# Optimization experiments

Measured on AMD Instinct MI355X. Metric: run time of the kernel, lower is better.

## Reference

```python
import jax, jax.numpy as jnp
import numpy as np

N_NODES = 1_000_000
N_EDGES = 16_000_000
NUM_GRAPHS = 64
LATENT = 128
LAMBDA_LAP = 0.1
LAMBDA_DRIFT = 0.01
LAMBDA_ARAP = 0.1
BETA_WARMUP = 10
BETA_FINAL = 1.0


def setup_inputs() -> dict:
    key = jax.random.key(0)
    k1, k2, k3, k4, k5, k6 = jax.random.split(key, 6)
    return {
        "pred_output": jax.random.normal(k1, (N_NODES, 2), dtype=jnp.float32),
        "target": jax.random.normal(k2, (N_NODES, 2), dtype=jnp.float32),
        "edge_index": jax.random.randint(k3, (2, N_EDGES), 0, N_NODES, dtype=jnp.int32),
        "batch_indices": jnp.sort(jax.random.randint(k4, (N_NODES,), 0, NUM_GRAPHS, dtype=jnp.int32)),
        "mu": jax.random.normal(k5, (NUM_GRAPHS, LATENT), dtype=jnp.float32),
        "logvar": jax.random.normal(k6, (NUM_GRAPHS, LATENT), dtype=jnp.float32),
        "epoch": 5,
    }


def reference(pred_output, target, edge_index, batch_indices, mu, logvar, epoch):
    # reconstruction: MSE, mean over all elements
    recon = jnp.mean((pred_output - target) ** 2)

    # edge gather once; laplacian and ARAP reuse the same diff tensor
    i, j = edge_index[0], edge_index[1]
    diff = pred_output[i] - pred_output[j]                 # [E, 2]
    lap = jnp.sum(diff ** 2) / edge_index.shape[1]

    # drift suppression: per-graph mean displacement via segment_sum
    ones = jnp.ones((pred_output.shape[0],), dtype=pred_output.dtype)
    sums = jax.ops.segment_sum(pred_output, batch_indices, num_segments=NUM_GRAPHS)
    counts = jax.ops.segment_sum(ones, batch_indices, num_segments=NUM_GRAPHS)
    means = sums / counts[:, None]                         # [G, 2]
    drift = jnp.sum(means ** 2) / NUM_GRAPHS

    # ARAP: unbiased variance of edge lengths (torch.var default ddof=1)
    edge_len = jnp.sqrt(jnp.sum(diff ** 2, axis=1))        # [E]
    arap = jnp.var(edge_len, ddof=1)

    # KL divergence, mean over graphs
    kl = jnp.mean(-0.5 * jnp.sum(1.0 + logvar - mu ** 2 - jnp.exp(logvar), axis=1))

    # beta warmup (epoch is a static python int)
    beta = (epoch / BETA_WARMUP) * BETA_FINAL if epoch < BETA_WARMUP else BETA_FINAL

    total = recon + LAMBDA_LAP * lap + LAMBDA_DRIFT * drift + LAMBDA_ARAP * arap + beta * kl
    return total
```

## Files before the change

kernel.cpp:

```cpp
#include <hip/hip_runtime.h>
#include <hip/hip_fp16.h>
#include <math.h>

#define N_NODES    1000000
#define N_EDGES    16000000
#define NUM_GRAPHS 64
#define LATENT     128

#define NODE_BLOCKS 512
#define EDGE_BLOCKS 2048

#define EDGE_PART_OFF  0
#define RECON_PART_OFF 32768
#define KL_PART_OFF    36864
#define GSUM_PART_OFF  36872
#define PACKED_OFF     458752
#define WS_NEEDED      (PACKED_OFF + 4ull * N_NODES)

typedef int vint4 __attribute__((ext_vector_type(4)));

__global__ void node_kl_pass(const float2* __restrict__ pred,
                             const float2* __restrict__ targ,
                             const int*    __restrict__ batch,
                             const float*  __restrict__ mu,
                             const float*  __restrict__ logvar,
                             double* __restrict__ recon_part,
                             double* __restrict__ kl_part,
                             float*  __restrict__ gsum_part,
                             unsigned* __restrict__ packed) {
    __shared__ float sgx[NUM_GRAPHS];
    __shared__ float sgy[NUM_GRAPHS];
    __shared__ int   scnt[NUM_GRAPHS];
    __shared__ double smem[8];

    for (int g = threadIdx.x; g < NUM_GRAPHS; g += blockDim.x) {
        sgx[g] = 0.f; sgy[g] = 0.f; scnt[g] = 0;
    }
    __syncthreads();

    float recon = 0.f;
    const int idx = blockIdx.x * blockDim.x + threadIdx.x;
    const int stride = gridDim.x * blockDim.x;
    for (int n = idx; n < N_NODES; n += stride) {
        float2 p = pred[n];
        float2 t = targ[n];
        float dx = p.x - t.x, dy = p.y - t.y;
        recon += dx * dx + dy * dy;

        if (packed) {
            __half2 h = __floats2half2_rn(p.x, p.y);
            packed[n] = *reinterpret_cast<unsigned*>(&h);
        }

        int b = batch[n];
        unsigned long long act = __ballot(1);
        int b0 = __shfl(b, 0);
        bool fast = (act == ~0ull) && (__ballot(b == b0) == act);
        if (fast) {
            float sx = p.x, sy = p.y;
            #pragma unroll
            for (int off = 32; off > 0; off >>= 1) {
                sx += __shfl_xor(sx, off);
                sy += __shfl_xor(sy, off);
            }
            if ((threadIdx.x & 63) == 0) {
                atomicAdd(&sgx[b0], sx);
                atomicAdd(&sgy[b0], sy);
                atomicAdd(&scnt[b0], 64);
            }
        } else {
            atomicAdd(&sgx[b], p.x);
            atomicAdd(&sgy[b], p.y);
            atomicAdd(&scnt[b], 1);
        }
    }

    double r = (double)recon;
    #pragma unroll
    for (int off = 32; off > 0; off >>= 1) r += __shfl_down(r, off);
    const int lane = threadIdx.x & 63;
    const int wid  = threadIdx.x >> 6;
    if (lane == 0) smem[wid] = r;
    __syncthreads();
    if (threadIdx.x == 0) {
        recon_part[blockIdx.x] = smem[0] + smem[1] + smem[2] + smem[3];
    }

    float* slot = gsum_part + (size_t)blockIdx.x * 192;
    for (int g = threadIdx.x; g < NUM_GRAPHS; g += blockDim.x) {
        slot[g]       = sgx[g];
        slot[64 + g]  = sgy[g];
        slot[128 + g] = (float)scnt[g];
    }

    if (blockIdx.x == 0) {
        double s = 0.0;
        for (int t = threadIdx.x; t < NUM_GRAPHS * LATENT; t += blockDim.x) {
            float m = mu[t], lv = logvar[t];
            s += (double)(1.0f + lv - m * m - expf(lv));
        }
        #pragma unroll
        for (int off = 32; off > 0; off >>= 1) s += __shfl_down(s, off);
        __syncthreads();
        if (lane == 0) smem[wid] = s;
        __syncthreads();
        if (threadIdx.x == 0) {
            kl_part[0] = smem[0] + smem[1] + smem[2] + smem[3];
        }
    }
}

__device__ __forceinline__ void edge_flush(float s1, float s2,
                                           double* __restrict__ edge_part,
                                           double* smem1, double* smem2) {
    double r1 = (double)s1, r2 = (double)s2;
    #pragma unroll
    for (int off = 32; off > 0; off >>= 1) {
        r1 += __shfl_down(r1, off);
        r2 += __shfl_down(r2, off);
    }
    const int lane = threadIdx.x & 63;
    const int wid  = threadIdx.x >> 6;
    if (lane == 0) { smem1[wid] = r1; smem2[wid] = r2; }
    __syncthreads();
    if (threadIdx.x == 0) {
        edge_part[2 * blockIdx.x]     = smem1[0] + smem1[1] + smem1[2] + smem1[3];
        edge_part[2 * blockIdx.x + 1] = smem2[0] + smem2[1] + smem2[2] + smem2[3];
    }
}

__global__ void edge_pass_packed(const unsigned* __restrict__ packed,
                                 const int* __restrict__ ei,
                                 double* __restrict__ edge_part) {
    __shared__ double smem1[8];
    __shared__ double smem2[8];

    float s1 = 0.f, s2 = 0.f;
    const int gid = blockIdx.x * blockDim.x + threadIdx.x;
    const int stride = gridDim.x * blockDim.x;
    const int ngroups = N_EDGES / 4;
    const vint4* eia = (const vint4*)ei;
    const vint4* eib = (const vint4*)(ei + N_EDGES);

    int g = gid;
    if (g < ngroups) {
        vint4 a = __builtin_nontemporal_load(eia + g);
        vint4 b = __builtin_nontemporal_load(eib + g);
        while (true) {
            unsigned pa0 = packed[a.x], pb0 = packed[b.x];
            unsigned pa1 = packed[a.y], pb1 = packed[b.y];
            unsigned pa2 = packed[a.z], pb2 = packed[b.z];
            unsigned pa3 = packed[a.w], pb3 = packed[b.w];

            const int gn = g + stride;
            const bool more = gn < ngroups;
            vint4 an = {0, 0, 0, 0}, bn = {0, 0, 0, 0};
            if (more) {
                an = __builtin_nontemporal_load(eia + gn);
                bn = __builtin_nontemporal_load(eib + gn);
            }

            {
                __half2 ha = *reinterpret_cast<__half2*>(&pa0);
                __half2 hb = *reinterpret_cast<__half2*>(&pb0);
                float2 fa = __half22float2(ha);
                float2 fb = __half22float2(hb);
                float dx = fa.x - fb.x, dy = fa.y - fb.y;
                float l2 = dx * dx + dy * dy;
                s2 += l2; s1 += sqrtf(l2);
            }
            {
                __half2 ha = *reinterpret_cast<__half2*>(&pa1);
                __half2 hb = *reinterpret_cast<__half2*>(&pb1);
                float2 fa = __half22float2(ha);
                float2 fb = __half22float2(hb);
                float dx = fa.x - fb.x, dy = fa.y - fb.y;
                float l2 = dx * dx + dy * dy;
                s2 += l2; s1 += sqrtf(l2);
            }
            {
                __half2 ha = *reinterpret_cast<__half2*>(&pa2);
                __half2 hb = *reinterpret_cast<__half2*>(&pb2);
                float2 fa = __half22float2(ha);
                float2 fb = __half22float2(hb);
                float dx = fa.x - fb.x, dy = fa.y - fb.y;
                float l2 = dx * dx + dy * dy;
                s2 += l2; s1 += sqrtf(l2);
            }
            {
                __half2 ha = *reinterpret_cast<__half2*>(&pa3);
                __half2 hb = *reinterpret_cast<__half2*>(&pb3);
                float2 fa = __half22float2(ha);
                float2 fb = __half22float2(hb);
                float dx = fa.x - fb.x, dy = fa.y - fb.y;
                float l2 = dx * dx + dy * dy;
                s2 += l2; s1 += sqrtf(l2);
            }

            if (!more) break;
            g = gn; a = an; b = bn;
        }
    }
    edge_flush(s1, s2, edge_part, smem1, smem2);
}

__global__ void edge_pass_f32(const float2* __restrict__ pred,
                              const int* __restrict__ ei,
                              double* __restrict__ edge_part) {
    __shared__ double smem1[8];
    __shared__ double smem2[8];

    float s1 = 0.f, s2 = 0.f;
    const int idx = blockIdx.x * blockDim.x + threadIdx.x;
    const int stride = gridDim.x * blockDim.x;
    for (int e = idx; e < N_EDGES; e += stride) {
        int i = ei[e];
        int j = ei[N_EDGES + e];
        float2 pi = pred[i];
        float2 pj = pred[j];
        float dx = pi.x - pj.x, dy = pi.y - pj.y;
        float l2 = dx * dx + dy * dy;
        s2 += l2;
        s1 += sqrtf(l2);
    }
    edge_flush(s1, s2, edge_part, smem1, smem2);
}

__device__ __forceinline__ double block_reduce_256(double v, double* sm) {
    #pragma unroll
    for (int off = 32; off > 0; off >>= 1) v += __shfl_down(v, off);
    const int lane = threadIdx.x & 63;
    const int wid  = threadIdx.x >> 6;
    __syncthreads();
    if (lane == 0) sm[wid] = v;
    __syncthreads();
    return sm[0] + sm[1] + sm[2] + sm[3];
}

__global__ void finalize(const double* __restrict__ edge_part,
                         const double* __restrict__ recon_part,
                         const double* __restrict__ kl_part,
                         const float*  __restrict__ gsum_part,
                         const int*    __restrict__ epoch_p,
                         float* __restrict__ out) {
    __shared__ double sx_s[256], sy_s[256], sc_s[256];
    __shared__ double sm[8];

    const int t = threadIdx.x;

    double reconv = 0.0;
    for (int b = t; b < NODE_BLOCKS; b += 256) reconv += recon_part[b];
    double s1 = 0.0, s2 = 0.0;
    for (int b = t; b < EDGE_BLOCKS; b += 256) {
        s1 += edge_part[2 * b];
        s2 += edge_part[2 * b + 1];
    }

    {
        const int g = t & 63, q = t >> 6;
        double gx = 0.0, gy = 0.0, gc = 0.0;
        for (int b = q; b < NODE_BLOCKS; b += 4) {
            const float* slot = gsum_part + (size_t)b * 192;
            gx += slot[g]; gy += slot[64 + g]; gc += slot[128 + g];
        }
        sx_s[t] = gx; sy_s[t] = gy; sc_s[t] = gc;
    }
    __syncthreads();

    double drift = 0.0;
    if (t < 64) {
        double X = sx_s[t] + sx_s[t + 64] + sx_s[t + 128] + sx_s[t + 192];
        double Y = sy_s[t] + sy_s[t + 64] + sy_s[t + 128] + sy_s[t + 192];
        double C = sc_s[t] + sc_s[t + 64] + sc_s[t + 128] + sc_s[t + 192];
        double mx = X / C, my = Y / C;
        drift = mx * mx + my * my;
    }
    #pragma unroll
    for (int off = 32; off > 0; off >>= 1) drift += __shfl_down(drift, off);

    reconv = block_reduce_256(reconv, sm);
    s1     = block_reduce_256(s1, sm);
    s2     = block_reduce_256(s2, sm);

    if (t == 0) {
        double recon = reconv / (2.0 * (double)N_NODES);
        double lap   = s2 / (double)N_EDGES;
        double arap  = (s2 - s1 * s1 / (double)N_EDGES) / ((double)N_EDGES - 1.0);
        double drft  = drift / (double)NUM_GRAPHS;
        double kl    = -0.5 * kl_part[0] / (double)NUM_GRAPHS;
        int epoch = *epoch_p;
        double beta = (epoch < 10) ? ((double)epoch / 10.0) : 1.0;
        out[0] = (float)(recon + 0.1 * lap + 0.01 * drft + 0.1 * arap + beta * kl);
    }
}

extern "C" void kernel_launch(void* const* d_in, const int* in_sizes, int n_in,
                              void* d_out, int out_size, void* d_ws, size_t ws_size,
                              hipStream_t stream) {
    const float2* pred   = (const float2*)d_in[0];
    const float2* targ   = (const float2*)d_in[1];
    const int*    ei     = (const int*)d_in[2];
    const int*    batch  = (const int*)d_in[3];
    const float*  mu     = (const float*)d_in[4];
    const float*  logvar = (const float*)d_in[5];
    const int*    epoch  = (const int*)d_in[6];
    float* out = (float*)d_out;

    char* ws = (char*)d_ws;
    double* edge_part  = (double*)(ws + EDGE_PART_OFF);
    double* recon_part = (double*)(ws + RECON_PART_OFF);
    double* kl_part    = (double*)(ws + KL_PART_OFF);
    float*  gsum_part  = (float*)(ws + GSUM_PART_OFF);

    const bool use_packed = ws_size >= WS_NEEDED;
    unsigned* packed = use_packed ? (unsigned*)(ws + PACKED_OFF) : (unsigned*)nullptr;

    node_kl_pass<<<NODE_BLOCKS, 256, 0, stream>>>(pred, targ, batch, mu, logvar,
                                                  recon_part, kl_part, gsum_part, packed);
    if (use_packed)
        edge_pass_packed<<<EDGE_BLOCKS, 256, 0, stream>>>(packed, ei, edge_part);
    else
        edge_pass_f32<<<EDGE_BLOCKS, 256, 0, stream>>>(pred, ei, edge_part);
    finalize<<<1, 256, 0, stream>>>(edge_part, recon_part, kl_part, gsum_part, epoch, out);
}
```

Before: 384.6 us.

## Fuse node, edge and finalize passes into one cooperative kernel with grid syncs

```diff
diff --git a/kernel.cpp b/kernel.cpp
--- a/kernel.cpp
+++ b/kernel.cpp
@@ -1,37 +1,47 @@
 #include <hip/hip_runtime.h>
+#include <hip/hip_cooperative_groups.h>
 #include <hip/hip_fp16.h>
 #include <math.h>
+
+namespace cg = cooperative_groups;
 
 #define N_NODES    1000000
 #define N_EDGES    16000000
 #define NUM_GRAPHS 64
 #define LATENT     128
-
-#define NODE_BLOCKS 512
-#define EDGE_BLOCKS 2048
+#define MAX_BLOCKS 2048
 
 #define EDGE_PART_OFF  0
 #define RECON_PART_OFF 32768
-#define KL_PART_OFF    36864
-#define GSUM_PART_OFF  36872
-#define PACKED_OFF     458752
+#define KL_PART_OFF    49152
+#define GSUM_PART_OFF  49216
+#define PACKED_OFF     2097152
 #define WS_NEEDED      (PACKED_OFF + 4ull * N_NODES)
 
 typedef int vint4 __attribute__((ext_vector_type(4)));
 
-__global__ void node_kl_pass(const float2* __restrict__ pred,
-                             const float2* __restrict__ targ,
-                             const int*    __restrict__ batch,
-                             const float*  __restrict__ mu,
-                             const float*  __restrict__ logvar,
-                             double* __restrict__ recon_part,
-                             double* __restrict__ kl_part,
-                             float*  __restrict__ gsum_part,
-                             unsigned* __restrict__ packed) {
+__global__ __launch_bounds__(256, 8)
+void fused_all(const float2* __restrict__ pred,
+               const float2* __restrict__ targ,
+               const int*    __restrict__ batch,
+               const float*  __restrict__ mu,
+               const float*  __restrict__ logvar,
+               const int*    __restrict__ ei,
+               const int*    __restrict__ epoch_p,
+               float*        __restrict__ out,
+               double* __restrict__ edge_part,
+               double* __restrict__ recon_part,
+               double* __restrict__ kl_part,
+               float*  __restrict__ gsum_part,
+               unsigned* __restrict__ packed) {
     __shared__ float sgx[NUM_GRAPHS];
     __shared__ float sgy[NUM_GRAPHS];
     __shared__ int   scnt[NUM_GRAPHS];
     __shared__ double smem[8];
+    __shared__ double sx_s[256], sy_s[256], sc_s[256];
+
+    const int lane = threadIdx.x & 63;
+    const int wid  = threadIdx.x >> 6;
 
     for (int g = threadIdx.x; g < NUM_GRAPHS; g += blockDim.x) {
         sgx[g] = 0.f; sgy[g] = 0.f; scnt[g] = 0;
@@ -47,10 +57,8 @@
         float dx = p.x - t.x, dy = p.y - t.y;
         recon += dx * dx + dy * dy;
 
-        if (packed) {
-            __half2 h = __floats2half2_rn(p.x, p.y);
-            packed[n] = *reinterpret_cast<unsigned*>(&h);
-        }
+        __half2 h = __floats2half2_rn(p.x, p.y);
+        packed[n] = *reinterpret_cast<unsigned*>(&h);
 
         int b = batch[n];
         unsigned long long act = __ballot(1);
@@ -63,7 +71,7 @@
                 sx += __shfl_xor(sx, off);
                 sy += __shfl_xor(sy, off);
             }
-            if ((threadIdx.x & 63) == 0) {
+            if (lane == 0) {
                 atomicAdd(&sgx[b0], sx);
                 atomicAdd(&sgy[b0], sy);
                 atomicAdd(&scnt[b0], 64);
@@ -78,13 +86,229 @@
     double r = (double)recon;
     #pragma unroll
     for (int off = 32; off > 0; off >>= 1) r += __shfl_down(r, off);
+    if (lane == 0) smem[wid] = r;
+    __syncthreads();
+    if (threadIdx.x == 0)
+        recon_part[blockIdx.x] = smem[0] + smem[1] + smem[2] + smem[3];
+
+    {
+        float* slot = gsum_part + (size_t)blockIdx.x * 192;
+        for (int g = threadIdx.x; g < NUM_GRAPHS; g += blockDim.x) {
+            slot[g]       = sgx[g];
+            slot[64 + g]  = sgy[g];
+            slot[128 + g] = (float)scnt[g];
+        }
+    }
+
+    if (blockIdx.x == 0) {
+        double s = 0.0;
+        for (int t = threadIdx.x; t < NUM_GRAPHS * LATENT; t += blockDim.x) {
+            float m = mu[t], lv = logvar[t];
+            s += (double)(1.0f + lv - m * m - expf(lv));
+        }
+        #pragma unroll
+        for (int off = 32; off > 0; off >>= 1) s += __shfl_down(s, off);
+        __syncthreads();
+        if (lane == 0) smem[wid] = s;
+        __syncthreads();
+        if (threadIdx.x == 0)
+            kl_part[0] = smem[0] + smem[1] + smem[2] + smem[3];
+    }
+
+    cg::this_grid().sync();
+
+    {
+        float s1 = 0.f, s2 = 0.f;
+        const int ngroups = N_EDGES / 4;
+        const vint4* eia = (const vint4*)ei;
+        const vint4* eib = (const vint4*)(ei + N_EDGES);
+
+        int g = idx;
+        if (g < ngroups) {
+            vint4 a = __builtin_nontemporal_load(eia + g);
+            vint4 b = __builtin_nontemporal_load(eib + g);
+            while (true) {
+                unsigned pa0 = packed[a.x], pb0 = packed[b.x];
+                unsigned pa1 = packed[a.y], pb1 = packed[b.y];
+                unsigned pa2 = packed[a.z], pb2 = packed[b.z];
+                unsigned pa3 = packed[a.w], pb3 = packed[b.w];
+
+                const int gn = g + stride;
+                const bool more = gn < ngroups;
+                vint4 an = {0, 0, 0, 0}, bn = {0, 0, 0, 0};
+                if (more) {
+                    an = __builtin_nontemporal_load(eia + gn);
+                    bn = __builtin_nontemporal_load(eib + gn);
+                }
+
+                {
+                    __half2 ha = *reinterpret_cast<__half2*>(&pa0);
+                    __half2 hb = *reinterpret_cast<__half2*>(&pb0);
+                    float2 fa = __half22float2(ha);
+                    float2 fb = __half22float2(hb);
+                    float dx = fa.x - fb.x, dy = fa.y - fb.y;
+                    float l2 = dx * dx + dy * dy;
+                    s2 += l2; s1 += sqrtf(l2);
+                }
+                {
+                    __half2 ha = *reinterpret_cast<__half2*>(&pa1);
+                    __half2 hb = *reinterpret_cast<__half2*>(&pb1);
+                    float2 fa = __half22float2(ha);
+                    float2 fb = __half22float2(hb);
+                    float dx = fa.x - fb.x, dy = fa.y - fb.y;
+                    float l2 = dx * dx + dy * dy;
+                    s2 += l2; s1 += sqrtf(l2);
+                }
+                {
+                    __half2 ha = *reinterpret_cast<__half2*>(&pa2);
+                    __half2 hb = *reinterpret_cast<__half2*>(&pb2);
+                    float2 fa = __half22float2(ha);
+                    float2 fb = __half22float2(hb);
+                    float dx = fa.x - fb.x, dy = fa.y - fb.y;
+                    float l2 = dx * dx + dy * dy;
+                    s2 += l2; s1 += sqrtf(l2);
+                }
+                {
+                    __half2 ha = *reinterpret_cast<__half2*>(&pa3);
+                    __half2 hb = *reinterpret_cast<__half2*>(&pb3);
+                    float2 fa = __half22float2(ha);
+                    float2 fb = __half22float2(hb);
+                    float dx = fa.x - fb.x, dy = fa.y - fb.y;
+                    float l2 = dx * dx + dy * dy;
+                    s2 += l2; s1 += sqrtf(l2);
+                }
+
+                if (!more) break;
+                g = gn; a = an; b = bn;
+            }
+        }
+
+        double r1 = (double)s1, r2 = (double)s2;
+        #pragma unroll
+        for (int off = 32; off > 0; off >>= 1) {
+            r1 += __shfl_down(r1, off);
+            r2 += __shfl_down(r2, off);
+        }
+        __syncthreads();
+        if (lane == 0) { smem[wid] = r1; smem[4 + wid] = r2; }
+        __syncthreads();
+        if (threadIdx.x == 0) {
+            edge_part[2 * blockIdx.x]     = smem[0] + smem[1] + smem[2] + smem[3];
+            edge_part[2 * blockIdx.x + 1] = smem[4] + smem[5] + smem[6] + smem[7];
+        }
+    }
+
+    cg::this_grid().sync();
+
+    if (blockIdx.x == 0) {
+        const int t = threadIdx.x;
+        const int NB = gridDim.x;
+
+        double reconv = 0.0;
+        for (int b = t; b < NB; b += 256) reconv += recon_part[b];
+        double s1 = 0.0, s2 = 0.0;
+        for (int b = t; b < NB; b += 256) {
+            s1 += edge_part[2 * b];
+            s2 += edge_part[2 * b + 1];
+        }
+
+        {
+            const int g = t & 63, q = t >> 6;
+            double gx = 0.0, gy = 0.0, gc = 0.0;
+            for (int b = q; b < NB; b += 4) {
+                const float* slot = gsum_part + (size_t)b * 192;
+                gx += slot[g]; gy += slot[64 + g]; gc += slot[128 + g];
+            }
+            sx_s[t] = gx; sy_s[t] = gy; sc_s[t] = gc;
+        }
+        __syncthreads();
+
+        double drift = 0.0;
+        if (t < 64) {
+            double X = sx_s[t] + sx_s[t + 64] + sx_s[t + 128] + sx_s[t + 192];
+            double Y = sy_s[t] + sy_s[t + 64] + sy_s[t + 128] + sy_s[t + 192];
+            double C = sc_s[t] + sc_s[t + 64] + sc_s[t + 128] + sc_s[t + 192];
+            double mx = X / C, my = Y / C;
+            drift = mx * mx + my * my;
+        }
+        #pragma unroll
+        for (int off = 32; off > 0; off >>= 1) drift += __shfl_down(drift, off);
+
+        #pragma unroll
+        for (int off = 32; off > 0; off >>= 1) reconv += __shfl_down(reconv, off);
+        __syncthreads();
+        if (lane == 0) smem[wid] = reconv;
+        __syncthreads();
+        reconv = smem[0] + smem[1] + smem[2] + smem[3];
+
+        #pragma unroll
+        for (int off = 32; off > 0; off >>= 1) s1 += __shfl_down(s1, off);
+        __syncthreads();
+        if (lane == 0) smem[wid] = s1;
+        __syncthreads();
+        s1 = smem[0] + smem[1] + smem[2] + smem[3];
+
+        #pragma unroll
+        for (int off = 32; off > 0; off >>= 1) s2 += __shfl_down(s2, off);
+        __syncthreads();
+        if (lane == 0) smem[wid] = s2;
+        __syncthreads();
+        s2 = smem[0] + smem[1] + smem[2] + smem[3];
+
+        if (t == 0) {
+            double recon = reconv / (2.0 * (double)N_NODES);
+            double lap   = s2 / (double)N_EDGES;
+            double arap  = (s2 - s1 * s1 / (double)N_EDGES) / ((double)N_EDGES - 1.0);
+            double drft  = drift / (double)NUM_GRAPHS;
+            double kl    = -0.5 * kl_part[0] / (double)NUM_GRAPHS;
+            int epoch = *epoch_p;
+            double beta = (epoch < 10) ? ((double)epoch / 10.0) : 1.0;
+            out[0] = (float)(recon + 0.1 * lap + 0.01 * drft + 0.1 * arap + beta * kl);
+        }
+    }
+}
+
+__global__ void node_kl_pass_fb(const float2* __restrict__ pred,
+                                const float2* __restrict__ targ,
+                                const int*    __restrict__ batch,
+                                const float*  __restrict__ mu,
+                                const float*  __restrict__ logvar,
+                                double* __restrict__ recon_part,
+                                double* __restrict__ kl_part,
+                                float*  __restrict__ gsum_part) {
+    __shared__ float sgx[NUM_GRAPHS];
+    __shared__ float sgy[NUM_GRAPHS];
+    __shared__ int   scnt[NUM_GRAPHS];
+    __shared__ double smem[8];
+
+    for (int g = threadIdx.x; g < NUM_GRAPHS; g += blockDim.x) {
+        sgx[g] = 0.f; sgy[g] = 0.f; scnt[g] = 0;
+    }
+    __syncthreads();
+
+    float recon = 0.f;
+    const int idx = blockIdx.x * blockDim.x + threadIdx.x;
+    const int stride = gridDim.x * blockDim.x;
+    for (int n = idx; n < N_NODES; n += stride) {
+        float2 p = pred[n];
+        float2 t = targ[n];
+        float dx = p.x - t.x, dy = p.y - t.y;
+        recon += dx * dx + dy * dy;
+        int b = batch[n];
+        atomicAdd(&sgx[b], p.x);
+        atomicAdd(&sgy[b], p.y);
+        atomicAdd(&scnt[b], 1);
+    }
+
+    double r = (double)recon;
+    #pragma unroll
+    for (int off = 32; off > 0; off >>= 1) r += __shfl_down(r, off);
     const int lane = threadIdx.x & 63;
     const int wid  = threadIdx.x >> 6;
     if (lane == 0) smem[wid] = r;
     __syncthreads();
-    if (threadIdx.x == 0) {
+    if (threadIdx.x == 0)
         recon_part[blockIdx.x] = smem[0] + smem[1] + smem[2] + smem[3];
-    }
 
     float* slot = gsum_part + (size_t)blockIdx.x * 192;
     for (int g = threadIdx.x; g < NUM_GRAPHS; g += blockDim.x) {
@@ -104,112 +328,16 @@
         __syncthreads();
         if (lane == 0) smem[wid] = s;
         __syncthreads();
-        if (threadIdx.x == 0) {
+        if (threadIdx.x == 0)
             kl_part[0] = smem[0] + smem[1] + smem[2] + smem[3];
-        }
     }
 }
 
-__device__ __forceinline__ void edge_flush(float s1, float s2,
-                                           double* __restrict__ edge_part,
-                                           double* smem1, double* smem2) {
-    double r1 = (double)s1, r2 = (double)s2;
-    #pragma unroll
-    for (int off = 32; off > 0; off >>= 1) {
-        r1 += __shfl_down(r1, off);
-        r2 += __shfl_down(r2, off);
-    }
-    const int lane = threadIdx.x & 63;
-    const int wid  = threadIdx.x >> 6;
-    if (lane == 0) { smem1[wid] = r1; smem2[wid] = r2; }
-    __syncthreads();
-    if (threadIdx.x == 0) {
-        edge_part[2 * blockIdx.x]     = smem1[0] + smem1[1] + smem1[2] + smem1[3];
-        edge_part[2 * blockIdx.x + 1] = smem2[0] + smem2[1] + smem2[2] + smem2[3];
-    }
-}
-
-__global__ void edge_pass_packed(const unsigned* __restrict__ packed,
+__global__ void edge_pass_f32_fb(const float2* __restrict__ pred,
                                  const int* __restrict__ ei,
                                  double* __restrict__ edge_part) {
     __shared__ double smem1[8];
     __shared__ double smem2[8];
-
-    float s1 = 0.f, s2 = 0.f;
-    const int gid = blockIdx.x * blockDim.x + threadIdx.x;
-    const int stride = gridDim.x * blockDim.x;
-    const int ngroups = N_EDGES / 4;
-    const vint4* eia = (const vint4*)ei;
-    const vint4* eib = (const vint4*)(ei + N_EDGES);
-
-    int g = gid;
-    if (g < ngroups) {
-        vint4 a = __builtin_nontemporal_load(eia + g);
-        vint4 b = __builtin_nontemporal_load(eib + g);
-        while (true) {
-            unsigned pa0 = packed[a.x], pb0 = packed[b.x];
-            unsigned pa1 = packed[a.y], pb1 = packed[b.y];
-            unsigned pa2 = packed[a.z], pb2 = packed[b.z];
-            unsigned pa3 = packed[a.w], pb3 = packed[b.w];
-
-            const int gn = g + stride;
-            const bool more = gn < ngroups;
-            vint4 an = {0, 0, 0, 0}, bn = {0, 0, 0, 0};
-            if (more) {
-                an = __builtin_nontemporal_load(eia + gn);
-                bn = __builtin_nontemporal_load(eib + gn);
-            }
-
-            {
-                __half2 ha = *reinterpret_cast<__half2*>(&pa0);
-                __half2 hb = *reinterpret_cast<__half2*>(&pb0);
-                float2 fa = __half22float2(ha);
-                float2 fb = __half22float2(hb);
-                float dx = fa.x - fb.x, dy = fa.y - fb.y;
-                float l2 = dx * dx + dy * dy;
-                s2 += l2; s1 += sqrtf(l2);
-            }
-            {
-                __half2 ha = *reinterpret_cast<__half2*>(&pa1);
-                __half2 hb = *reinterpret_cast<__half2*>(&pb1);
-                float2 fa = __half22float2(ha);
-                float2 fb = __half22float2(hb);
-                float dx = fa.x - fb.x, dy = fa.y - fb.y;
-                float l2 = dx * dx + dy * dy;
-                s2 += l2; s1 += sqrtf(l2);
-            }
-            {
-                __half2 ha = *reinterpret_cast<__half2*>(&pa2);
-                __half2 hb = *reinterpret_cast<__half2*>(&pb2);
-                float2 fa = __half22float2(ha);
-                float2 fb = __half22float2(hb);
-                float dx = fa.x - fb.x, dy = fa.y - fb.y;
-                float l2 = dx * dx + dy * dy;
-                s2 += l2; s1 += sqrtf(l2);
-            }
-            {
-                __half2 ha = *reinterpret_cast<__half2*>(&pa3);
-                __half2 hb = *reinterpret_cast<__half2*>(&pb3);
-                float2 fa = __half22float2(ha);
-                float2 fb = __half22float2(hb);
-                float dx = fa.x - fb.x, dy = fa.y - fb.y;
-                float l2 = dx * dx + dy * dy;
-                s2 += l2; s1 += sqrtf(l2);
-            }
-
-            if (!more) break;
-            g = gn; a = an; b = bn;
-        }
-    }
-    edge_flush(s1, s2, edge_part, smem1, smem2);
-}
-
-__global__ void edge_pass_f32(const float2* __restrict__ pred,
-                              const int* __restrict__ ei,
-                              double* __restrict__ edge_part) {
-    __shared__ double smem1[8];
-    __shared__ double smem2[8];
-
     float s1 = 0.f, s2 = 0.f;
     const int idx = blockIdx.x * blockDim.x + threadIdx.x;
     const int stride = gridDim.x * blockDim.x;
@@ -223,43 +351,44 @@
         s2 += l2;
         s1 += sqrtf(l2);
     }
-    edge_flush(s1, s2, edge_part, smem1, smem2);
-}
-
-__device__ __forceinline__ double block_reduce_256(double v, double* sm) {
-    #pragma unroll
-    for (int off = 32; off > 0; off >>= 1) v += __shfl_down(v, off);
+    double r1 = (double)s1, r2 = (double)s2;
+    #pragma unroll
+    for (int off = 32; off > 0; off >>= 1) {
+        r1 += __shfl_down(r1, off);
+        r2 += __shfl_down(r2, off);
+    }
     const int lane = threadIdx.x & 63;
     const int wid  = threadIdx.x >> 6;
-    __syncthreads();
-    if (lane == 0) sm[wid] = v;
-    __syncthreads();
-    return sm[0] + sm[1] + sm[2] + sm[3];
+    if (lane == 0) { smem1[wid] = r1; smem2[wid] = r2; }
+    __syncthreads();
+    if (threadIdx.x == 0) {
+        edge_part[2 * blockIdx.x]     = smem1[0] + smem1[1] + smem1[2] + smem1[3];
+        edge_part[2 * blockIdx.x + 1] = smem2[0] + smem2[1] + smem2[2] + smem2[3];
+    }
 }
 
-__global__ void finalize(const double* __restrict__ edge_part,
-                         const double* __restrict__ recon_part,
-                         const double* __restrict__ kl_part,
-                         const float*  __restrict__ gsum_part,
-                         const int*    __restrict__ epoch_p,
-                         float* __restrict__ out) {
+__global__ void finalize_fb(const double* __restrict__ edge_part, int n_edge_blocks,
+                            const double* __restrict__ recon_part, int n_node_blocks,
+                            const double* __restrict__ kl_part,
+                            const float*  __restrict__ gsum_part,
+                            const int*    __restrict__ epoch_p,
+                            float* __restrict__ out) {
     __shared__ double sx_s[256], sy_s[256], sc_s[256];
     __shared__ double sm[8];
-
     const int t = threadIdx.x;
+    const int lane = t & 63, wid = t >> 6;
 
     double reconv = 0.0;
-    for (int b = t; b < NODE_BLOCKS; b += 256) reconv += recon_part[b];
+    for (int b = t; b < n_node_blocks; b += 256) reconv += recon_part[b];
     double s1 = 0.0, s2 = 0.0;
-    for (int b = t; b < EDGE_BLOCKS; b += 256) {
+    for (int b = t; b < n_edge_blocks; b += 256) {
         s1 += edge_part[2 * b];
         s2 += edge_part[2 * b + 1];
     }
-
     {
         const int g = t & 63, q = t >> 6;
         double gx = 0.0, gy = 0.0, gc = 0.0;
-        for (int b = q; b < NODE_BLOCKS; b += 4) {
+        for (int b = q; b < n_node_blocks; b += 4) {
             const float* slot = gsum_part + (size_t)b * 192;
             gx += slot[g]; gy += slot[64 + g]; gc += slot[128 + g];
         }
@@ -278,9 +407,18 @@
     #pragma unroll
     for (int off = 32; off > 0; off >>= 1) drift += __shfl_down(drift, off);
 
-    reconv = block_reduce_256(reconv, sm);
-    s1     = block_reduce_256(s1, sm);
-    s2     = block_reduce_256(s2, sm);
+    #pragma unroll
+    for (int off = 32; off > 0; off >>= 1) reconv += __shfl_down(reconv, off);
+    __syncthreads(); if (lane == 0) sm[wid] = reconv; __syncthreads();
+    reconv = sm[0] + sm[1] + sm[2] + sm[3];
+    #pragma unroll
+    for (int off = 32; off > 0; off >>= 1) s1 += __shfl_down(s1, off);
+    __syncthreads(); if (lane == 0) sm[wid] = s1; __syncthreads();
+    s1 = sm[0] + sm[1] + sm[2] + sm[3];
+    #pragma unroll
+    for (int off = 32; off > 0; off >>= 1) s2 += __shfl_down(s2, off);
+    __syncthreads(); if (lane == 0) sm[wid] = s2; __syncthreads();
+    s2 = sm[0] + sm[1] + sm[2] + sm[3];
 
     if (t == 0) {
         double recon = reconv / (2.0 * (double)N_NODES);
@@ -311,15 +449,28 @@
     double* recon_part = (double*)(ws + RECON_PART_OFF);
     double* kl_part    = (double*)(ws + KL_PART_OFF);
     float*  gsum_part  = (float*)(ws + GSUM_PART_OFF);
-
-    const bool use_packed = ws_size >= WS_NEEDED;
-    unsigned* packed = use_packed ? (unsigned*)(ws + PACKED_OFF) : (unsigned*)nullptr;
-
-    node_kl_pass<<<NODE_BLOCKS, 256, 0, stream>>>(pred, targ, batch, mu, logvar,
-                                                  recon_part, kl_part, gsum_part, packed);
-    if (use_packed)
-        edge_pass_packed<<<EDGE_BLOCKS, 256, 0, stream>>>(packed, ei, edge_part);
-    else
-        edge_pass_f32<<<EDGE_BLOCKS, 256, 0, stream>>>(pred, ei, edge_part);
-    finalize<<<1, 256, 0, stream>>>(edge_part, recon_part, kl_part, gsum_part, epoch, out);
+    unsigned* packed   = (unsigned*)(ws + PACKED_OFF);
+
+    if (ws_size >= WS_NEEDED) {
+        int maxb = 0;
+        if (hipOccupancyMaxActiveBlocksPerMultiprocessor(
+                &maxb, reinterpret_cast<const void*>(&fused_all), 256, 0) != hipSuccess ||
+            maxb <= 0)
+            maxb = 4;
+        int grid = maxb * 256;
+        if (grid > MAX_BLOCKS) grid = MAX_BLOCKS;
+
+        void* args[] = {(void*)&pred, (void*)&targ, (void*)&batch, (void*)&mu,
+                        (void*)&logvar, (void*)&ei, (void*)&epoch, (void*)&out,
+                        (void*)&edge_part, (void*)&recon_part, (void*)&kl_part,
+                        (void*)&gsum_part, (void*)&packed};
+        hipLaunchCooperativeKernel(reinterpret_cast<const void*>(&fused_all),
+                                   dim3(grid), dim3(256), args, 0, stream);
+    } else {
+        node_kl_pass_fb<<<512, 256, 0, stream>>>(pred, targ, batch, mu, logvar,
+                                                 recon_part, kl_part, gsum_part);
+        edge_pass_f32_fb<<<MAX_BLOCKS, 256, 0, stream>>>(pred, ei, edge_part);
+        finalize_fb<<<1, 256, 0, stream>>>(edge_part, MAX_BLOCKS, recon_part, 512,
+                                           kl_part, gsum_part, epoch, out);
+    }
 }
```

New measurement: 794.3 us. +106.5%, slower.
